# Optimization experiments

Hardware: AMD Instinct MI355X
Metric: run time of the kernel (lower is better)

The kernel has to match this reference:

```python
import jax, jax.numpy as jnp
import numpy as np

B, F, D_IN, H, OUT = 32768, 200, 5, 15, 30

def setup_inputs() -> dict:
    key = jax.random.key(0)
    ks = jax.random.split(key, 7)
    return {
        "y":  jax.random.normal(ks[0], (B, F, D_IN), dtype=jnp.float32),
        "W1": jax.random.normal(ks[1], (F, D_IN, H), dtype=jnp.float32) * 0.3,
        "b1": jax.random.normal(ks[2], (F, H), dtype=jnp.float32) * 0.1,
        "W2": jax.random.normal(ks[3], (F, H, OUT), dtype=jnp.float32) * 0.2,
        "b2": jax.random.normal(ks[4], (F, OUT), dtype=jnp.float32) * 0.1,
        "W3": jax.random.normal(ks[5], (F * OUT, 1), dtype=jnp.float32) * 0.02,
        "b3": jax.random.normal(ks[6], (1,), dtype=jnp.float32) * 0.1,
    }

def reference(y, W1, b1, W2, b2, W3, b3):
    # 200 independent tiny 2-layer MLPs, batched over the feature axis f.
    # Note: original applies ReLU only AFTER the second Linear.
    h1 = jnp.einsum('bfi,fih->bfh', y, W1) + b1          # [B, F, H]
    h2 = jax.nn.relu(jnp.einsum('bfh,fho->bfo', h1, W2) + b2)  # [B, F, OUT]
    flat = h2.reshape(h2.shape[0], -1)                   # concat along feature axis -> [B, F*OUT]
    return flat @ W3 + b3                                # [B, 1]
```

## Files before the change

kernel.cpp:

```cpp
#include <hip/hip_runtime.h>

#define B_TOTAL 32768
#define NF 200
#define D_IN 5
#define NH 15
#define NOUT 30

typedef _Float16 half8 __attribute__((ext_vector_type(8)));
typedef _Float16 half4_t __attribute__((ext_vector_type(4)));
typedef float f32x4 __attribute__((ext_vector_type(4)));
typedef float f32x2 __attribute__((ext_vector_type(2)));

#define WS_BC_BYTES 102400
#define WS_TOTAL (102400 + 30720)

#define GPF 8

__global__ __launch_bounds__(256) void precompute_kernel(
    const float* __restrict__ W1, const float* __restrict__ b1,
    const float* __restrict__ W2, const float* __restrict__ b2,
    const float* __restrict__ W3, _Float16* __restrict__ Bc,
    float* __restrict__ w3T, float* __restrict__ out)
{
    __shared__ __align__(16) float sW1[GPF * 75];
    __shared__ __align__(16) float sW2[GPF * 450];
    __shared__ __align__(16) float sb1[GPF * 15];
    __shared__ __align__(16) float sb2[GPF * 30];
    __shared__ __align__(16) float sW3[GPF * 30];

    const int tid = threadIdx.x;
    const int f0  = blockIdx.x * GPF;

    {
        const f32x4 z4 = {0.f, 0.f, 0.f, 0.f};
        for (int j = blockIdx.x * 256 + tid; j < B_TOTAL / 4; j += 25 * 256)
            ((f32x4*)out)[j] = z4;
    }

    {
        const f32x4* g1 = (const f32x4*)(W1 + (size_t)f0 * 75);
        if (tid < 150) ((f32x4*)sW1)[tid] = g1[tid];
        const f32x4* g2 = (const f32x4*)(W2 + (size_t)f0 * 450);
        for (int j = tid; j < 900; j += 256) ((f32x4*)sW2)[j] = g2[j];
        if (tid < 30)
            ((f32x4*)sb1)[tid] = ((const f32x4*)(b1 + (size_t)f0 * 15))[tid];
        if (tid >= 32 && tid < 92)
            ((f32x4*)sb2)[tid - 32] = ((const f32x4*)(b2 + (size_t)f0 * 30))[tid - 32];
        if (tid >= 96 && tid < 156)
            ((f32x4*)sW3)[tid - 96] = ((const f32x4*)(W3 + (size_t)f0 * 30))[tid - 96];
    }
    __syncthreads();

    const int fi = tid >> 5;
    const int r  = tid & 31;
    const int hf = r >> 4;
    const int n  = r & 15;
    const int o  = hf * 16 + n;
    const int f  = f0 + fi;

    half8 row = {};
    if (o < NOUT) {
        float bcv = sb2[fi * 30 + o];
        float wc0 = 0.f, wc1 = 0.f, wc2 = 0.f, wc3 = 0.f, wc4 = 0.f;
        #pragma unroll
        for (int h = 0; h < NH; ++h) {
            const float w2v = sW2[fi * 450 + h * 30 + o];
            bcv = fmaf(sb1[fi * 15 + h], w2v, bcv);
            wc0 = fmaf(sW1[fi * 75 +  0 + h], w2v, wc0);
            wc1 = fmaf(sW1[fi * 75 + 15 + h], w2v, wc1);
            wc2 = fmaf(sW1[fi * 75 + 30 + h], w2v, wc2);
            wc3 = fmaf(sW1[fi * 75 + 45 + h], w2v, wc3);
            wc4 = fmaf(sW1[fi * 75 + 60 + h], w2v, wc4);
        }
        row[0] = (_Float16)wc0; row[1] = (_Float16)wc1; row[2] = (_Float16)wc2;
        row[3] = (_Float16)wc3; row[4] = (_Float16)wc4;
        row[5] = (_Float16)bcv;
        row[6] = (_Float16)0.f; row[7] = (_Float16)0.f;

        const int p = f / 20, fl = f % 20, Kg = fl / 4, w = fl % 4;
        w3T[((size_t)(p * 4 + w) * 16 + n) * 12 + (Kg * 2 + hf)] = sW3[fi * 30 + o];
    }
    *(half8*)(Bc + (size_t)f * 256 + r * 8) = row;
}

#define FPART 20
#define NPARTS 10

__global__ __launch_bounds__(256, 4) void mlp_kernel(
    const float* __restrict__ y, const _Float16* __restrict__ Bc,
    const float* __restrict__ w3T, const float* __restrict__ b3,
    float* __restrict__ out)
{
    __shared__ __align__(16) _Float16 sy[64 * 168];
    __shared__ __align__(16) _Float16 sB[20 * 256];
    __shared__ __align__(16) float    sw3[4 * 16 * 12];
    __shared__ __align__(16) _Float16 szero[8];

    const int tid = threadIdx.x;
    const int b0  = blockIdx.x * 64;
    const int p   = blockIdx.y;
    const int f0  = p * FPART;

    if (tid < 8) szero[tid] = (_Float16)0.f;
    {
        const f32x4* g = (const f32x4*)(Bc + (size_t)f0 * 256);
        f32x4* s = (f32x4*)sB;
        s[tid]       = g[tid];
        s[tid + 256] = g[tid + 256];
        if (tid < 128) s[tid + 512] = g[tid + 512];
    }
    if (tid < 192) ((f32x4*)sw3)[tid] = ((const f32x4*)w3T)[(size_t)p * 192 + tid];
    #pragma unroll
    for (int it = 0; it < 5; ++it) {
        const int id = tid + it * 256;
        const int b  = id / 20;
        const int fl = id - b * 20;
        const float* src = y + (size_t)(b0 + b) * (NF * D_IN) + (size_t)(f0 + fl) * 5;
        float v[5];
        __builtin_memcpy(v, src, 20);
        half8 h;
        h[0] = (_Float16)v[0]; h[1] = (_Float16)v[1]; h[2] = (_Float16)v[2];
        h[3] = (_Float16)v[3]; h[4] = (_Float16)v[4];
        h[5] = (_Float16)1.0f; h[6] = (_Float16)0.f; h[7] = (_Float16)0.f;
        *(half8*)&sy[b * 168 + fl * 8] = h;
    }
    __syncthreads();

    const int lane = tid & 63;
    const int w    = tid >> 6;
    const int n    = lane & 15;
    const int q    = lane >> 4;

    float acc[4][4];
    #pragma unroll
    for (int Mt = 0; Mt < 4; ++Mt)
        #pragma unroll
        for (int g = 0; g < 4; ++g) acc[Mt][g] = 0.f;
    const f32x4 z4 = {0.f, 0.f, 0.f, 0.f};

    #pragma unroll 1
    for (int Kg = 0; Kg < 5; ++Kg) {
        const int fl = Kg * 4 + w;
        half4_t A[4];
        #pragma unroll
        for (int Mt = 0; Mt < 4; ++Mt)
            A[Mt] = *(const half4_t*)&sy[(Mt * 16 + n) * 168 + fl * 8 + (q & 1) * 4];

        const _Float16* bq0 = (q < 2) ? &sB[fl * 256 + n * 8 + (q & 1) * 4]        : szero;
        const _Float16* bq1 = (q < 2) ? &sB[fl * 256 + (16 + n) * 8 + (q & 1) * 4] : szero;
        const half4_t Bf0 = *(const half4_t*)bq0;
        const half4_t Bf1 = *(const half4_t*)bq1;

        const f32x2 w3p = *(const f32x2*)&sw3[(w * 16 + n) * 12 + Kg * 2];
        const float w30 = w3p[0], w31 = w3p[1];

        #pragma unroll
        for (int Mt = 0; Mt < 4; ++Mt) {
            f32x4 c0 = __builtin_amdgcn_mfma_f32_16x16x16f16(A[Mt], Bf0, z4, 0, 0, 0);
            f32x4 c1 = __builtin_amdgcn_mfma_f32_16x16x16f16(A[Mt], Bf1, z4, 0, 0, 0);
            #pragma unroll
            for (int g = 0; g < 4; ++g)
                acc[Mt][g] += fmaxf(c0[g], 0.f) * w30 + fmaxf(c1[g], 0.f) * w31;
        }
    }

    __syncthreads();
    float* sacc = (float*)sy;
    {
        float* base = sacc + w * (64 * 20);
        #pragma unroll
        for (int Mt = 0; Mt < 4; ++Mt)
            #pragma unroll
            for (int g = 0; g < 4; ++g)
                base[(Mt * 16 + q * 4 + g) * 20 + n] = acc[Mt][g];
    }
    const float* srow = sacc + w * (64 * 20) + lane * 20;
    f32x4 r0 = *(const f32x4*)(srow);
    f32x4 r1 = *(const f32x4*)(srow + 4);
    f32x4 r2 = *(const f32x4*)(srow + 8);
    f32x4 r3 = *(const f32x4*)(srow + 12);
    float v = ((r0[0] + r0[1]) + (r0[2] + r0[3]))
            + ((r1[0] + r1[1]) + (r1[2] + r1[3]))
            + ((r2[0] + r2[1]) + (r2[2] + r2[3]))
            + ((r3[0] + r3[1]) + (r3[2] + r3[3]));
    float* sp = (float*)sB;
    sp[w * 64 + lane] = v;
    __syncthreads();
    if (tid < 64) {
        float s = (sp[tid] + sp[64 + tid]) + (sp[128 + tid] + sp[192 + tid]);
        if (p == 0) s += b3[0];
        atomicAdd(&out[b0 + tid], s);
    }
}

extern "C" void kernel_launch(void* const* d_in, const int* in_sizes, int n_in,
                              void* d_out, int out_size, void* d_ws, size_t ws_size,
                              hipStream_t stream) {
    const float* y  = (const float*)d_in[0];
    const float* W1 = (const float*)d_in[1];
    const float* b1 = (const float*)d_in[2];
    const float* W2 = (const float*)d_in[3];
    const float* b2 = (const float*)d_in[4];
    const float* W3 = (const float*)d_in[5];
    const float* b3 = (const float*)d_in[6];
    float* out = (float*)d_out;

    _Float16* Bc  = (_Float16*)d_ws;
    float*    w3T = (float*)((char*)d_ws + WS_BC_BYTES);

    precompute_kernel<<<NF / GPF, 256, 0, stream>>>(W1, b1, W2, b2, W3, Bc, w3T, out);
    mlp_kernel<<<dim3(B_TOTAL / 64, NPARTS), 256, 0, stream>>>(y, Bc, w3T, b3, out);
}
```

Baseline: 208.6 us.

## Loop over feature partitions in-block with register prefetch, drop atomics

Each block now handles 32 batch rows across all 10 feature partitions. It loops over the partitions and prefetches the next partition's y, Bc and w3 slices into registers while the MFMA work runs on the current one. The 10 partial sums no longer go through atomicAdd, so the output is written directly and the precompute kernel stops zeroing it. In exchange the grid has fewer, longer blocks, each with less batch parallelism, extra syncthreads per partition, and higher register pressure from the prefetch buffers.

After: 292.7 us. +40.3%, slower.

```diff
diff --git a/kernel.cpp b/kernel.cpp
--- a/kernel.cpp
+++ b/kernel.cpp
@@ -12,7 +12,6 @@
 typedef float f32x2 __attribute__((ext_vector_type(2)));
 
 #define WS_BC_BYTES 102400
-#define WS_TOTAL (102400 + 30720)
 
 #define GPF 8
 
@@ -20,7 +19,7 @@
     const float* __restrict__ W1, const float* __restrict__ b1,
     const float* __restrict__ W2, const float* __restrict__ b2,
     const float* __restrict__ W3, _Float16* __restrict__ Bc,
-    float* __restrict__ w3T, float* __restrict__ out)
+    float* __restrict__ w3T)
 {
     __shared__ __align__(16) float sW1[GPF * 75];
     __shared__ __align__(16) float sW2[GPF * 450];
@@ -30,12 +29,6 @@
 
     const int tid = threadIdx.x;
     const int f0  = blockIdx.x * GPF;
-
-    {
-        const f32x4 z4 = {0.f, 0.f, 0.f, 0.f};
-        for (int j = blockIdx.x * 256 + tid; j < B_TOTAL / 4; j += 25 * 256)
-            ((f32x4*)out)[j] = z4;
-    }
 
     {
         const f32x4* g1 = (const f32x4*)(W1 + (size_t)f0 * 75);
@@ -85,111 +78,149 @@
 
 #define FPART 20
 #define NPARTS 10
+#define BTILE 32
 
 __global__ __launch_bounds__(256, 4) void mlp_kernel(
     const float* __restrict__ y, const _Float16* __restrict__ Bc,
     const float* __restrict__ w3T, const float* __restrict__ b3,
     float* __restrict__ out)
 {
-    __shared__ __align__(16) _Float16 sy[64 * 168];
+    __shared__ __align__(16) _Float16 sy[BTILE * 168];
     __shared__ __align__(16) _Float16 sB[20 * 256];
-    __shared__ __align__(16) float    sw3[4 * 16 * 12];
+    __shared__ __align__(16) float    sw3[768];
     __shared__ __align__(16) _Float16 szero[8];
 
     const int tid = threadIdx.x;
-    const int b0  = blockIdx.x * 64;
-    const int p   = blockIdx.y;
-    const int f0  = p * FPART;
+    const int b0  = blockIdx.x * BTILE;
 
     if (tid < 8) szero[tid] = (_Float16)0.f;
+
+    const int bt0 = tid / 20,             flt0 = tid - bt0 * 20;
+    const int id1 = tid + 256;  const int bt1 = id1 / 20, flt1 = id1 - bt1 * 20;
+    const int id2 = tid + 512;  const int bt2 = id2 / 20, flt2 = id2 - bt2 * 20;
+    const bool has2 = (tid < 128);
+    const bool hasw = (tid < 192);
+
+    float vy0[5], vy1[5], vy2[5];
+    f32x4 vB0, vB1, vB2, vw;
+
+    const float* ybase = y + (size_t)b0 * (NF * D_IN);
+
     {
+        const int f0 = 0;
+        __builtin_memcpy(vy0, ybase + (size_t)bt0 * (NF * D_IN) + (f0 + flt0) * 5, 20);
+        __builtin_memcpy(vy1, ybase + (size_t)bt1 * (NF * D_IN) + (f0 + flt1) * 5, 20);
+        if (has2)
+            __builtin_memcpy(vy2, ybase + (size_t)bt2 * (NF * D_IN) + (f0 + flt2) * 5, 20);
         const f32x4* g = (const f32x4*)(Bc + (size_t)f0 * 256);
-        f32x4* s = (f32x4*)sB;
-        s[tid]       = g[tid];
-        s[tid + 256] = g[tid + 256];
-        if (tid < 128) s[tid + 512] = g[tid + 512];
-    }
-    if (tid < 192) ((f32x4*)sw3)[tid] = ((const f32x4*)w3T)[(size_t)p * 192 + tid];
-    #pragma unroll
-    for (int it = 0; it < 5; ++it) {
-        const int id = tid + it * 256;
-        const int b  = id / 20;
-        const int fl = id - b * 20;
-        const float* src = y + (size_t)(b0 + b) * (NF * D_IN) + (size_t)(f0 + fl) * 5;
-        float v[5];
-        __builtin_memcpy(v, src, 20);
-        half8 h;
-        h[0] = (_Float16)v[0]; h[1] = (_Float16)v[1]; h[2] = (_Float16)v[2];
-        h[3] = (_Float16)v[3]; h[4] = (_Float16)v[4];
-        h[5] = (_Float16)1.0f; h[6] = (_Float16)0.f; h[7] = (_Float16)0.f;
-        *(half8*)&sy[b * 168 + fl * 8] = h;
-    }
-    __syncthreads();
+        vB0 = g[tid]; vB1 = g[tid + 256];
+        if (has2) vB2 = g[tid + 512];
+        if (hasw) vw = ((const f32x4*)w3T)[tid];
+    }
 
     const int lane = tid & 63;
     const int w    = tid >> 6;
     const int n    = lane & 15;
     const int q    = lane >> 4;
 
-    float acc[4][4];
+    float acc[2][4];
     #pragma unroll
-    for (int Mt = 0; Mt < 4; ++Mt)
+    for (int Mt = 0; Mt < 2; ++Mt)
         #pragma unroll
         for (int g = 0; g < 4; ++g) acc[Mt][g] = 0.f;
     const f32x4 z4 = {0.f, 0.f, 0.f, 0.f};
 
     #pragma unroll 1
-    for (int Kg = 0; Kg < 5; ++Kg) {
-        const int fl = Kg * 4 + w;
-        half4_t A[4];
-        #pragma unroll
-        for (int Mt = 0; Mt < 4; ++Mt)
-            A[Mt] = *(const half4_t*)&sy[(Mt * 16 + n) * 168 + fl * 8 + (q & 1) * 4];
-
-        const _Float16* bq0 = (q < 2) ? &sB[fl * 256 + n * 8 + (q & 1) * 4]        : szero;
-        const _Float16* bq1 = (q < 2) ? &sB[fl * 256 + (16 + n) * 8 + (q & 1) * 4] : szero;
-        const half4_t Bf0 = *(const half4_t*)bq0;
-        const half4_t Bf1 = *(const half4_t*)bq1;
-
-        const f32x2 w3p = *(const f32x2*)&sw3[(w * 16 + n) * 12 + Kg * 2];
-        const float w30 = w3p[0], w31 = w3p[1];
-
-        #pragma unroll
-        for (int Mt = 0; Mt < 4; ++Mt) {
-            f32x4 c0 = __builtin_amdgcn_mfma_f32_16x16x16f16(A[Mt], Bf0, z4, 0, 0, 0);
-            f32x4 c1 = __builtin_amdgcn_mfma_f32_16x16x16f16(A[Mt], Bf1, z4, 0, 0, 0);
-            #pragma unroll
-            for (int g = 0; g < 4; ++g)
-                acc[Mt][g] += fmaxf(c0[g], 0.f) * w30 + fmaxf(c1[g], 0.f) * w31;
+    for (int p = 0; p < NPARTS; ++p) {
+        __syncthreads();
+        {
+            half8 h;
+            h[0]=(_Float16)vy0[0]; h[1]=(_Float16)vy0[1]; h[2]=(_Float16)vy0[2];
+            h[3]=(_Float16)vy0[3]; h[4]=(_Float16)vy0[4];
+            h[5]=(_Float16)1.0f;   h[6]=(_Float16)0.f;    h[7]=(_Float16)0.f;
+            *(half8*)&sy[bt0 * 168 + flt0 * 8] = h;
+            h[0]=(_Float16)vy1[0]; h[1]=(_Float16)vy1[1]; h[2]=(_Float16)vy1[2];
+            h[3]=(_Float16)vy1[3]; h[4]=(_Float16)vy1[4];
+            h[5]=(_Float16)1.0f;
+            *(half8*)&sy[bt1 * 168 + flt1 * 8] = h;
+            if (has2) {
+                h[0]=(_Float16)vy2[0]; h[1]=(_Float16)vy2[1]; h[2]=(_Float16)vy2[2];
+                h[3]=(_Float16)vy2[3]; h[4]=(_Float16)vy2[4];
+                h[5]=(_Float16)1.0f;
+                *(half8*)&sy[bt2 * 168 + flt2 * 8] = h;
+            }
+            f32x4* s = (f32x4*)sB;
+            s[tid] = vB0; s[tid + 256] = vB1;
+            if (has2) s[tid + 512] = vB2;
+            if (hasw) ((f32x4*)sw3)[tid] = vw;
+        }
+        __syncthreads();
+        if (p + 1 < NPARTS) {
+            const int f0 = (p + 1) * FPART;
+            __builtin_memcpy(vy0, ybase + (size_t)bt0 * (NF * D_IN) + (f0 + flt0) * 5, 20);
+            __builtin_memcpy(vy1, ybase + (size_t)bt1 * (NF * D_IN) + (f0 + flt1) * 5, 20);
+            if (has2)
+                __builtin_memcpy(vy2, ybase + (size_t)bt2 * (NF * D_IN) + (f0 + flt2) * 5, 20);
+            const f32x4* g = (const f32x4*)(Bc + (size_t)f0 * 256);
+            vB0 = g[tid]; vB1 = g[tid + 256];
+            if (has2) vB2 = g[tid + 512];
+            if (hasw) vw = ((const f32x4*)w3T)[(size_t)(p + 1) * 192 + tid];
+        }
+        #pragma unroll
+        for (int Kg = 0; Kg < 5; ++Kg) {
+            const int fl = Kg * 4 + w;
+            const half4_t A0 = *(const half4_t*)&sy[n        * 168 + fl * 8 + (q & 1) * 4];
+            const half4_t A1 = *(const half4_t*)&sy[(16 + n) * 168 + fl * 8 + (q & 1) * 4];
+            const _Float16* bq0 = (q < 2) ? &sB[fl * 256 + n * 8 + (q & 1) * 4]        : szero;
+            const _Float16* bq1 = (q < 2) ? &sB[fl * 256 + (16 + n) * 8 + (q & 1) * 4] : szero;
+            const half4_t Bf0 = *(const half4_t*)bq0;
+            const half4_t Bf1 = *(const half4_t*)bq1;
+            const f32x2 w3p = *(const f32x2*)&sw3[(w * 16 + n) * 12 + Kg * 2];
+
+            f32x4 c;
+            c = __builtin_amdgcn_mfma_f32_16x16x16f16(A0, Bf0, z4, 0, 0, 0);
+            #pragma unroll
+            for (int g = 0; g < 4; ++g) acc[0][g] += fmaxf(c[g], 0.f) * w3p[0];
+            c = __builtin_amdgcn_mfma_f32_16x16x16f16(A0, Bf1, z4, 0, 0, 0);
+            #pragma unroll
+            for (int g = 0; g < 4; ++g) acc[0][g] += fmaxf(c[g], 0.f) * w3p[1];
+            c = __builtin_amdgcn_mfma_f32_16x16x16f16(A1, Bf0, z4, 0, 0, 0);
+            #pragma unroll
+            for (int g = 0; g < 4; ++g) acc[1][g] += fmaxf(c[g], 0.f) * w3p[0];
+            c = __builtin_amdgcn_mfma_f32_16x16x16f16(A1, Bf1, z4, 0, 0, 0);
+            #pragma unroll
+            for (int g = 0; g < 4; ++g) acc[1][g] += fmaxf(c[g], 0.f) * w3p[1];
         }
     }
 
     __syncthreads();
     float* sacc = (float*)sy;
     {
-        float* base = sacc + w * (64 * 20);
-        #pragma unroll
-        for (int Mt = 0; Mt < 4; ++Mt)
+        float* base = sacc + w * (32 * 20);
+        #pragma unroll
+        for (int Mt = 0; Mt < 2; ++Mt)
             #pragma unroll
             for (int g = 0; g < 4; ++g)
                 base[(Mt * 16 + q * 4 + g) * 20 + n] = acc[Mt][g];
     }
-    const float* srow = sacc + w * (64 * 20) + lane * 20;
-    f32x4 r0 = *(const f32x4*)(srow);
-    f32x4 r1 = *(const f32x4*)(srow + 4);
-    f32x4 r2 = *(const f32x4*)(srow + 8);
-    f32x4 r3 = *(const f32x4*)(srow + 12);
-    float v = ((r0[0] + r0[1]) + (r0[2] + r0[3]))
-            + ((r1[0] + r1[1]) + (r1[2] + r1[3]))
-            + ((r2[0] + r2[1]) + (r2[2] + r2[3]))
-            + ((r3[0] + r3[1]) + (r3[2] + r3[3]));
+    float v = 0.f;
+    if (lane < 32) {
+        const float* srow = sacc + w * (32 * 20) + lane * 20;
+        const f32x4 r0 = *(const f32x4*)(srow);
+        const f32x4 r1 = *(const f32x4*)(srow + 4);
+        const f32x4 r2 = *(const f32x4*)(srow + 8);
+        const f32x4 r3 = *(const f32x4*)(srow + 12);
+        v = ((r0[0] + r0[1]) + (r0[2] + r0[3]))
+          + ((r1[0] + r1[1]) + (r1[2] + r1[3]))
+          + ((r2[0] + r2[1]) + (r2[2] + r2[3]))
+          + ((r3[0] + r3[1]) + (r3[2] + r3[3]));
+    }
     float* sp = (float*)sB;
-    sp[w * 64 + lane] = v;
+    if (lane < 32) sp[w * 32 + lane] = v;
     __syncthreads();
-    if (tid < 64) {
-        float s = (sp[tid] + sp[64 + tid]) + (sp[128 + tid] + sp[192 + tid]);
-        if (p == 0) s += b3[0];
-        atomicAdd(&out[b0 + tid], s);
+    if (tid < 32) {
+        const float s = (sp[tid] + sp[32 + tid]) + (sp[64 + tid] + sp[96 + tid]) + b3[0];
+        out[b0 + tid] = s;
     }
 }
 
@@ -208,6 +239,6 @@
     _Float16* Bc  = (_Float16*)d_ws;
     float*    w3T = (float*)((char*)d_ws + WS_BC_BYTES);
 
-    precompute_kernel<<<NF / GPF, 256, 0, stream>>>(W1, b1, W2, b2, W3, Bc, w3T, out);
-    mlp_kernel<<<dim3(B_TOTAL / 64, NPARTS), 256, 0, stream>>>(y, Bc, w3T, b3, out);
+    precompute_kernel<<<NF / GPF, 256, 0, stream>>>(W1, b1, W2, b2, W3, Bc, w3T);
+    mlp_kernel<<<B_TOTAL / BTILE, 256, 0, stream>>>(y, Bc, w3T, b3, out);
 }
```
